# Kernel tuning notes

Measured on AMD Instinct MI355X. Metric: run time of the kernel, lower is better.

## Reference

```python
import jax, jax.numpy as jnp
import numpy as np

NUM_DIM = 512
NUM_STEPS = 20
TEMPERATURE = 1.0


def sinkhorn(matrix, num_steps):
    # Iterative log-space row/column normalization (Mena et al., 2018).
    S = matrix
    for _ in range(num_steps):
        S = S - jax.nn.logsumexp(S, axis=1, keepdims=True)  # row normalize
        S = S - jax.nn.logsumexp(S, axis=0, keepdims=True)  # column normalize
    return jnp.exp(S)


def setup_inputs() -> dict:
    key = jax.random.key(0)
    kx, kw = jax.random.split(key)
    x = jax.random.normal(kx, (NUM_DIM, 65536), dtype=jnp.float32)
    weight = jax.random.normal(kw, (NUM_DIM, NUM_DIM), dtype=jnp.float32)
    return {"x": x, "weight": weight}


def reference(x, weight):
    # doubly_stochastic_matrix = Sinkhorn(weight / temperature)
    dsm = sinkhorn(weight / TEMPERATURE, NUM_STEPS)  # [num_dim, num_dim]
    # x has num_dim as its first axis (dim_idx == 0) -> DSM @ x
    return dsm @ x  # [num_dim, N]
```

## Files before the change

kernel.cpp:

```cpp
#include <hip/hip_runtime.h>

typedef unsigned short ushort_t;
typedef float  f4v  __attribute__((ext_vector_type(4)));
typedef __bf16 bf4v __attribute__((ext_vector_type(4)));
typedef __bf16 bf8v __attribute__((ext_vector_type(8)));
typedef ushort_t us4 __attribute__((ext_vector_type(4)));

#define NDIM 512
#define NCOL 65536
#define NSTEPS 20

__device__ __forceinline__ ushort_t f2bf(float f) {
  unsigned u = __float_as_uint(f);
  u = (u + 0x7fffu + ((u >> 16) & 1u)) >> 16;
  return (ushort_t)u;
}
__device__ __forceinline__ float bf2f(ushort_t h) {
  return __uint_as_float(((unsigned)h) << 16);
}

__global__ void transpose_k(const float* __restrict__ W, float* __restrict__ WT,
                            float* __restrict__ r, float* __restrict__ c) {
  __shared__ float tile[32][33];
  if (blockIdx.x == 0 && blockIdx.y == 0) {
    r[threadIdx.x] = 0.f; r[threadIdx.x + 256] = 0.f;
    c[threadIdx.x] = 0.f; c[threadIdx.x + 256] = 0.f;
  }
  int bx = blockIdx.x * 32, by = blockIdx.y * 32;
  int tx = threadIdx.x & 31, ty = threadIdx.x >> 5;
#pragma unroll
  for (int i = 0; i < 32; i += 8)
    tile[ty + i][tx] = W[(size_t)(by + ty + i) * NDIM + bx + tx];
  __syncthreads();
#pragma unroll
  for (int i = 0; i < 32; i += 8)
    WT[(size_t)(bx + ty + i) * NDIM + by + tx] = tile[tx][ty + i];
}

__global__ void lse_step(const float* __restrict__ M, const float* __restrict__ sub,
                         float* __restrict__ dst) {
  int lane = threadIdx.x & 63;
  int wave = threadIdx.x >> 6;
  int row = blockIdx.x * 8 + wave;
  const f4v* mr = (const f4v*)(M + (size_t)row * NDIM);
  const f4v* sp = (const f4v*)sub;
  f4v a = mr[lane];
  f4v b = mr[lane + 64];
  f4v sa = sp[lane];
  f4v sb = sp[lane + 64];
  float v[8];
  v[0] = a[0] - sa[0]; v[1] = a[1] - sa[1]; v[2] = a[2] - sa[2]; v[3] = a[3] - sa[3];
  v[4] = b[0] - sb[0]; v[5] = b[1] - sb[1]; v[6] = b[2] - sb[2]; v[7] = b[3] - sb[3];
  float m = v[0];
#pragma unroll
  for (int i = 1; i < 8; ++i) m = fmaxf(m, v[i]);
#pragma unroll
  for (int off = 32; off > 0; off >>= 1) m = fmaxf(m, __shfl_xor(m, off));
  float s = 0.f;
#pragma unroll
  for (int i = 0; i < 8; ++i) s += expf(v[i] - m);
#pragma unroll
  for (int off = 32; off > 0; off >>= 1) s += __shfl_xor(s, off);
  if (lane == 0) dst[row] = m + logf(s);
}

__global__ void dsm_split(const float* __restrict__ W, const float* __restrict__ r,
                          const float* __restrict__ c, ushort_t* __restrict__ Ahi,
                          ushort_t* __restrict__ Alo) {
  int idx = blockIdx.x * 256 + threadIdx.x;
  int m = idx >> 7;
  int kq = idx & 127;
  f4v w = ((const f4v*)(W + (size_t)m * NDIM))[kq];
  f4v cc = ((const f4v*)c)[kq];
  float rm = r[m];
  us4 vh, vl;
#pragma unroll
  for (int i = 0; i < 4; ++i) {
    float v = expf(w[i] - rm - cc[i]);
    ushort_t h = f2bf(v);
    float res = v - bf2f(h);
    vh[i] = h;
    vl[i] = f2bf(res);
  }
  size_t base = (size_t)m * NDIM + kq * 4;
  *(us4*)(Ahi + base) = vh;
  *(us4*)(Alo + base) = vl;
}

__global__ __launch_bounds__(256, 2) void gemm_k(const float* __restrict__ X,
                                                 const ushort_t* __restrict__ Ahi,
                                                 const ushort_t* __restrict__ Alo,
                                                 float* __restrict__ out) {
  __shared__ ushort_t sBhi[128 * 32];
  __shared__ ushort_t sBlo[128 * 32];

  int bid = blockIdx.x;
  int swz = (bid & 7) * 256 + (bid >> 3);
  int nt = swz >> 2;
  int mt = swz & 3;

  int tid = threadIdx.x;
  int lane = tid & 63;
  int w = tid >> 6;
  int wr = w >> 1, wc = w & 1;

  int n4 = tid & 31;
  int fs_w = (n4 & 7) << 2;

  const ushort_t* Abase_hi =
      Ahi + (size_t)(mt * 128 + wr * 64 + (lane & 15)) * NDIM + (lane >> 4) * 8;
  const ushort_t* Abase_lo =
      Alo + (size_t)(mt * 128 + wr * 64 + (lane & 15)) * NDIM + (lane >> 4) * 8;

  f4v acc[4][4];
#pragma unroll
  for (int i = 0; i < 4; ++i)
#pragma unroll
    for (int j = 0; j < 4; ++j) acc[i][j] = (f4v)0.f;

  for (int kt = 0; kt < 16; ++kt) {
#pragma unroll
    for (int it = 0; it < 2; ++it) {
      int kp = (tid >> 5) + it * 8;
      int k = kp * 2;
      const f4v* p0 = (const f4v*)(X + (size_t)(kt * 32 + k) * NCOL + nt * 128) + n4;
      const f4v* p1 = (const f4v*)(X + (size_t)(kt * 32 + k + 1) * NCOL + nt * 128) + n4;
      f4v va = *p0;
      f4v vb = *p1;
#pragma unroll
      for (int cx = 0; cx < 4; ++cx) {
        int nn = n4 * 4 + cx;
        float x0 = va[cx], x1 = vb[cx];
        ushort_t h0 = f2bf(x0), h1 = f2bf(x1);
        float r0 = x0 - bf2f(h0), r1 = x1 - bf2f(h1);
        ushort_t l0 = f2bf(r0), l1 = f2bf(r1);
        int idx2 = nn * 32 + (k ^ fs_w);
        *(unsigned*)(&sBhi[idx2]) = (unsigned)h0 | ((unsigned)h1 << 16);
        *(unsigned*)(&sBlo[idx2]) = (unsigned)l0 | ((unsigned)l1 << 16);
      }
    }
    __syncthreads();

    bf8v ah[4], al[4];
#pragma unroll
    for (int i = 0; i < 4; ++i) {
      ah[i] = *(const bf8v*)(Abase_hi + (size_t)i * 16 * NDIM + kt * 32);
      al[i] = *(const bf8v*)(Abase_lo + (size_t)i * 16 * NDIM + kt * 32);
    }
    bf8v bh[4], bl[4];
#pragma unroll
    for (int j = 0; j < 4; ++j) {
      int nn = wc * 64 + j * 16 + (lane & 15);
      int fs = ((nn >> 2) & 7) << 2;
      int kc = (lane >> 4) * 8;
      int ia = nn * 32 + (kc ^ fs);
      int ib = nn * 32 + ((kc + 4) ^ fs);
      bf4v h0 = *(const bf4v*)(&sBhi[ia]);
      bf4v h1 = *(const bf4v*)(&sBhi[ib]);
      bf4v q0 = *(const bf4v*)(&sBlo[ia]);
      bf4v q1 = *(const bf4v*)(&sBlo[ib]);
      bf8v bhv, blv;
#pragma unroll
      for (int e = 0; e < 4; ++e) {
        bhv[e] = h0[e];
        bhv[e + 4] = h1[e];
        blv[e] = q0[e];
        blv[e + 4] = q1[e];
      }
      bh[j] = bhv;
      bl[j] = blv;
    }

#pragma unroll
    for (int i = 0; i < 4; ++i)
#pragma unroll
      for (int j = 0; j < 4; ++j) {
        acc[i][j] = __builtin_amdgcn_mfma_f32_16x16x32_bf16(ah[i], bh[j], acc[i][j], 0, 0, 0);
        acc[i][j] = __builtin_amdgcn_mfma_f32_16x16x32_bf16(ah[i], bl[j], acc[i][j], 0, 0, 0);
        acc[i][j] = __builtin_amdgcn_mfma_f32_16x16x32_bf16(al[i], bh[j], acc[i][j], 0, 0, 0);
      }
    __syncthreads();
  }

  float* outp = out + (size_t)(mt * 128 + wr * 64 + (lane >> 4) * 4) * NCOL + nt * 128 +
                wc * 64 + (lane & 15);
#pragma unroll
  for (int i = 0; i < 4; ++i)
#pragma unroll
    for (int j = 0; j < 4; ++j)
#pragma unroll
      for (int rr = 0; rr < 4; ++rr)
        outp[(size_t)(i * 16 + rr) * NCOL + j * 16] = acc[i][j][rr];
}

extern "C" void kernel_launch(void* const* d_in, const int* in_sizes, int n_in,
                              void* d_out, int out_size, void* d_ws, size_t ws_size,
                              hipStream_t stream) {
  const float* X = (const float*)d_in[0];
  const float* W = (const float*)d_in[1];
  float* out = (float*)d_out;

  float* r = (float*)d_ws;
  float* c = r + NDIM;
  float* WT = c + NDIM;
  ushort_t* Ahi = (ushort_t*)(WT + NDIM * NDIM);
  ushort_t* Alo = Ahi + NDIM * NDIM;

  transpose_k<<<dim3(16, 16), 256, 0, stream>>>(W, WT, r, c);
  for (int it = 0; it < NSTEPS; ++it) {
    lse_step<<<64, 512, 0, stream>>>(W, c, r);
    lse_step<<<64, 512, 0, stream>>>(WT, r, c);
  }
  dsm_split<<<256, 256, 0, stream>>>(W, r, c, Ahi, Alo);
  gemm_k<<<2048, 256, 0, stream>>>(X, Ahi, Alo, out);
}
```

Before: 474.0 us.

## Fuse Sinkhorn launches into one persistent kernel and prefetch X in GEMM

```diff
diff --git a/kernel.cpp b/kernel.cpp
--- a/kernel.cpp
+++ b/kernel.cpp
@@ -9,6 +9,8 @@
 #define NDIM 512
 #define NCOL 65536
 #define NSTEPS 20
+#define NBLK 64
+#define NBAR 41
 
 __device__ __forceinline__ ushort_t f2bf(float f) {
   unsigned u = __float_as_uint(f);
@@ -19,29 +21,28 @@
   return __uint_as_float(((unsigned)h) << 16);
 }
 
-__global__ void transpose_k(const float* __restrict__ W, float* __restrict__ WT,
-                            float* __restrict__ r, float* __restrict__ c) {
-  __shared__ float tile[32][33];
-  if (blockIdx.x == 0 && blockIdx.y == 0) {
-    r[threadIdx.x] = 0.f; r[threadIdx.x + 256] = 0.f;
-    c[threadIdx.x] = 0.f; c[threadIdx.x + 256] = 0.f;
-  }
-  int bx = blockIdx.x * 32, by = blockIdx.y * 32;
-  int tx = threadIdx.x & 31, ty = threadIdx.x >> 5;
-#pragma unroll
-  for (int i = 0; i < 32; i += 8)
-    tile[ty + i][tx] = W[(size_t)(by + ty + i) * NDIM + bx + tx];
+__device__ __forceinline__ void gbar(int* __restrict__ bar, int idx) {
   __syncthreads();
-#pragma unroll
-  for (int i = 0; i < 32; i += 8)
-    WT[(size_t)(bx + ty + i) * NDIM + by + tx] = tile[tx][ty + i];
-}
-
-__global__ void lse_step(const float* __restrict__ M, const float* __restrict__ sub,
-                         float* __restrict__ dst) {
-  int lane = threadIdx.x & 63;
-  int wave = threadIdx.x >> 6;
-  int row = blockIdx.x * 8 + wave;
+  __threadfence();
+  if (threadIdx.x == 0) {
+    atomicAdd(&bar[idx], 1);
+    while (atomicAdd(&bar[idx], 0) < NBLK) __builtin_amdgcn_s_sleep(2);
+  }
+  __syncthreads();
+  __threadfence();
+}
+
+__global__ void init_k(float* __restrict__ r, float* __restrict__ c,
+                       int* __restrict__ bar) {
+  int t = threadIdx.x;
+  r[t] = 0.f;
+  c[t] = 0.f;
+  if (t < 64) bar[t] = 0;
+}
+
+__device__ __forceinline__ void lse_row(const float* __restrict__ M,
+                                        const float* __restrict__ sub,
+                                        float* __restrict__ dst, int row, int lane) {
   const f4v* mr = (const f4v*)(M + (size_t)row * NDIM);
   const f4v* sp = (const f4v*)sub;
   f4v a = mr[lane];
@@ -64,30 +65,70 @@
   if (lane == 0) dst[row] = m + logf(s);
 }
 
-__global__ void dsm_split(const float* __restrict__ W, const float* __restrict__ r,
-                          const float* __restrict__ c, ushort_t* __restrict__ Ahi,
-                          ushort_t* __restrict__ Alo) {
-  int idx = blockIdx.x * 256 + threadIdx.x;
-  int m = idx >> 7;
-  int kq = idx & 127;
-  f4v w = ((const f4v*)(W + (size_t)m * NDIM))[kq];
-  f4v cc = ((const f4v*)c)[kq];
-  float rm = r[m];
-  us4 vh, vl;
-#pragma unroll
-  for (int i = 0; i < 4; ++i) {
-    float v = expf(w[i] - rm - cc[i]);
-    ushort_t h = f2bf(v);
-    float res = v - bf2f(h);
-    vh[i] = h;
-    vl[i] = f2bf(res);
-  }
-  size_t base = (size_t)m * NDIM + kq * 4;
-  *(us4*)(Ahi + base) = vh;
-  *(us4*)(Alo + base) = vl;
-}
-
-__global__ __launch_bounds__(256, 2) void gemm_k(const float* __restrict__ X,
+__global__ __launch_bounds__(512, 1) void sinkhorn_manual(
+    const float* __restrict__ W, float* __restrict__ WT, float* __restrict__ r,
+    float* __restrict__ c, ushort_t* __restrict__ Ahi, ushort_t* __restrict__ Alo,
+    int* __restrict__ bar) {
+  const int tid = threadIdx.x;
+  const int bid = blockIdx.x;
+
+  {
+    __shared__ float tile[4][32][33];
+    int sub = tid >> 7;
+    int t2 = tid & 127;
+    int tx = t2 & 31, tg = t2 >> 5;
+    int tindex = bid * 4 + sub;
+    int by = (tindex >> 4) * 32;
+    int bx = (tindex & 15) * 32;
+#pragma unroll
+    for (int i = 0; i < 8; ++i) {
+      int row = tg * 8 + i;
+      tile[sub][row][tx] = W[(size_t)(by + row) * NDIM + bx + tx];
+    }
+    __syncthreads();
+#pragma unroll
+    for (int i = 0; i < 8; ++i) {
+      int row = tg * 8 + i;
+      WT[(size_t)(bx + row) * NDIM + by + tx] = tile[sub][tx][row];
+    }
+  }
+  gbar(bar, 0);
+
+  int lane = tid & 63;
+  int wave = tid >> 6;
+  int row = bid * 8 + wave;
+  for (int it = 0; it < NSTEPS; ++it) {
+    lse_row(W, c, r, row, lane);
+    gbar(bar, 1 + 2 * it);
+    lse_row(WT, r, c, row, lane);
+    gbar(bar, 2 + 2 * it);
+  }
+
+  int gidx = bid * 512 + tid;
+#pragma unroll
+  for (int q = 0; q < 2; ++q) {
+    int idx = gidx * 2 + q;
+    int m = idx >> 7;
+    int kq = idx & 127;
+    f4v w = ((const f4v*)(W + (size_t)m * NDIM))[kq];
+    f4v cc = ((const f4v*)c)[kq];
+    float rm = r[m];
+    us4 vh, vl;
+#pragma unroll
+    for (int i = 0; i < 4; ++i) {
+      float v = expf(w[i] - rm - cc[i]);
+      ushort_t h = f2bf(v);
+      float res = v - bf2f(h);
+      vh[i] = h;
+      vl[i] = f2bf(res);
+    }
+    size_t base = (size_t)m * NDIM + kq * 4;
+    *(us4*)(Ahi + base) = vh;
+    *(us4*)(Alo + base) = vl;
+  }
+}
+
+__global__ __launch_bounds__(256, 3) void gemm_k(const float* __restrict__ X,
                                                  const ushort_t* __restrict__ Ahi,
                                                  const ushort_t* __restrict__ Alo,
                                                  float* __restrict__ out) {
@@ -106,6 +147,7 @@
 
   int n4 = tid & 31;
   int fs_w = (n4 & 7) << 2;
+  int kbase = (tid >> 5) * 2;
 
   const ushort_t* Abase_hi =
       Ahi + (size_t)(mt * 128 + wr * 64 + (lane & 15)) * NDIM + (lane >> 4) * 8;
@@ -118,19 +160,23 @@
 #pragma unroll
     for (int j = 0; j < 4; ++j) acc[i][j] = (f4v)0.f;
 
+  f4v va[2], vb[2];
+#pragma unroll
+  for (int it = 0; it < 2; ++it) {
+    int k = kbase + it * 16;
+    va[it] = *((const f4v*)(X + (size_t)k * NCOL + nt * 128) + n4);
+    vb[it] = *((const f4v*)(X + (size_t)(k + 1) * NCOL + nt * 128) + n4);
+  }
+
   for (int kt = 0; kt < 16; ++kt) {
 #pragma unroll
     for (int it = 0; it < 2; ++it) {
-      int kp = (tid >> 5) + it * 8;
-      int k = kp * 2;
-      const f4v* p0 = (const f4v*)(X + (size_t)(kt * 32 + k) * NCOL + nt * 128) + n4;
-      const f4v* p1 = (const f4v*)(X + (size_t)(kt * 32 + k + 1) * NCOL + nt * 128) + n4;
-      f4v va = *p0;
-      f4v vb = *p1;
+      int k = kbase + it * 16;
+      f4v xa = va[it], xb = vb[it];
 #pragma unroll
       for (int cx = 0; cx < 4; ++cx) {
         int nn = n4 * 4 + cx;
-        float x0 = va[cx], x1 = vb[cx];
+        float x0 = xa[cx], x1 = xb[cx];
         ushort_t h0 = f2bf(x0), h1 = f2bf(x1);
         float r0 = x0 - bf2f(h0), r1 = x1 - bf2f(h1);
         ushort_t l0 = f2bf(r0), l1 = f2bf(r1);
@@ -140,6 +186,16 @@
       }
     }
     __syncthreads();
+
+    if (kt < 15) {
+#pragma unroll
+      for (int it = 0; it < 2; ++it) {
+        int k = kbase + it * 16;
+        const float* base = X + (size_t)((kt + 1) * 32 + k) * NCOL + nt * 128;
+        va[it] = *((const f4v*)base + n4);
+        vb[it] = *((const f4v*)(base + NCOL) + n4);
+      }
+    }
 
     bf8v ah[4], al[4];
 #pragma unroll
@@ -205,12 +261,9 @@
   float* WT = c + NDIM;
   ushort_t* Ahi = (ushort_t*)(WT + NDIM * NDIM);
   ushort_t* Alo = Ahi + NDIM * NDIM;
-
-  transpose_k<<<dim3(16, 16), 256, 0, stream>>>(W, WT, r, c);
-  for (int it = 0; it < NSTEPS; ++it) {
-    lse_step<<<64, 512, 0, stream>>>(W, c, r);
-    lse_step<<<64, 512, 0, stream>>>(WT, r, c);
-  }
-  dsm_split<<<256, 256, 0, stream>>>(W, r, c, Ahi, Alo);
+  int* bar = (int*)(Alo + NDIM * NDIM);
+
+  init_k<<<1, 512, 0, stream>>>(r, c, bar);
+  sinkhorn_manual<<<NBLK, 512, 0, stream>>>(W, WT, r, c, Ahi, Alo, bar);
   gemm_k<<<2048, 256, 0, stream>>>(X, Ahi, Alo, out);
 }
```

New measurement: 1.032 ms. 118% more time.
